# Kernel optimization log

Measured on AMD Instinct MI355X. Metric: run time of the kernel, lower is better.

Reference implementation:

```python
import jax, jax.numpy as jnp
import numpy as np
import math

B, L, E, H, D = 2, 2048, 2048, 16, 128
LOGIT_SCALE_MAX = math.log(1.0 / 0.01)
EPS = 1e-6


def rms_norm(x, scale, eps=EPS):
    # UIOLayerNorm: no mean subtraction, no bias, fp32 internals
    x32 = x.astype(jnp.float32)
    ms = jnp.mean(x32 * x32, axis=-1, keepdims=True)
    return (scale * (x32 * jax.lax.rsqrt(ms + eps)).astype(x.dtype)).astype(x.dtype)


def apply_rotary(x, rope):
    # x: [b, l, h, d]; rope: [b, l, d] interpreted as (cos, sin) interleaved pairs
    b, l, h, d = x.shape
    xr = x.astype(jnp.float32).reshape(b, l, h, d // 2, 2)
    rc = rope.astype(jnp.float32).reshape(b, l, 1, d // 2, 2)
    out = jnp.stack(
        [xr[..., 0] * rc[..., 0] - xr[..., 1] * rc[..., 1],
         xr[..., 1] * rc[..., 0] + xr[..., 0] * rc[..., 1]], axis=-1)
    return out.reshape(b, l, h, d).astype(x.dtype)


def l2_normalize(x, eps=1e-12):
    # matches F.normalize(dim=-1): x / max(||x||, eps)
    n = jnp.sqrt(jnp.sum(x * x, axis=-1, keepdims=True))
    return x / jnp.maximum(n, eps)


def setup_inputs() -> dict:
    key = jax.random.key(0)
    ks = jax.random.split(key, 12)
    scale = 1.0 / math.sqrt(E)
    return {
        "inputs_q": jax.random.normal(ks[0], (B, L, E), jnp.float32),
        "inputs_kv": jax.random.normal(ks[1], (B, L, E), jnp.float32),
        "bias": jax.random.normal(ks[2], (1, 1, L, L), jnp.float32),
        "q_sinusoids": jax.random.uniform(ks[3], (B, L, D), jnp.float32, -1.0, 1.0),
        "k_sinusoids": jax.random.uniform(ks[4], (B, L, D), jnp.float32, -1.0, 1.0),
        "Wq": jax.random.normal(ks[5], (E, E), jnp.float32) * scale,
        "Wk": jax.random.normal(ks[6], (E, E), jnp.float32) * scale,
        "Wv": jax.random.normal(ks[7], (E, E), jnp.float32) * scale,
        "Wo": jax.random.normal(ks[8], (E, E), jnp.float32) * scale,
        "q_norm_scale": jnp.ones((D,), jnp.float32),
        "k_norm_scale": jnp.ones((D,), jnp.float32),
        "logit_scale": jnp.full((H,), math.log(10.0), jnp.float32),
    }


def reference(inputs_q, inputs_kv, bias, q_sinusoids, k_sinusoids,
              Wq, Wk, Wv, Wo, q_norm_scale, k_norm_scale, logit_scale):
    dtype = inputs_q.dtype
    b, ql, e = inputs_q.shape
    kl = inputs_kv.shape[1]
    # QKV projections (nn.Linear, no bias), split heads -> [b, len, h, d]
    q = (inputs_q @ Wq.T).reshape(b, ql, H, D)
    k = (inputs_kv @ Wk.T).reshape(b, kl, H, D)
    v = (inputs_kv @ Wv.T).reshape(b, kl, H, D)
    # qk_norm (UIO RMS norm over head_dim)
    q = rms_norm(q, q_norm_scale)
    k = rms_norm(k, k_norm_scale)
    # RoPE
    q = apply_rotary(q, q_sinusoids)
    k = apply_rotary(k, k_sinusoids)
    # float32_logits
    q32 = q.astype(jnp.float32)
    k32 = k.astype(jnp.float32)
    # scaled cosine attention: L2-normalize q,k; learned per-head logit scale
    scores = jnp.einsum("bqhd,bkhd->bhqk", l2_normalize(q32), l2_normalize(k32))
    ls = jnp.exp(jnp.minimum(logit_scale, LOGIT_SCALE_MAX))
    scores = scores * ls[None, :, None, None]
    scores = scores + bias.astype(scores.dtype)
    attn = jax.nn.softmax(scores, axis=-1).astype(dtype)
    out = jnp.einsum("bhqk,bkhd->bqhd", attn, v)
    out = out.reshape(b, ql, e)
    return out @ Wo.T
```

## Files before the change

### kernel.cpp

```cpp
#include <hip/hip_runtime.h>
#include <hip/hip_bf16.h>

#define B_ 2
#define L_ 2048
#define E_ 2048
#define H_ 16
#define D_ 128
#define M_ (B_*L_)
#define LOGIT_SCALE_MAX_ 4.6051701859880914f
#define LOG2E_ 1.44269504088896f

typedef __bf16 bf16_t;
typedef __bf16 bf16x2 __attribute__((ext_vector_type(2)));
typedef __bf16 bf16x4 __attribute__((ext_vector_type(4)));
typedef __bf16 bf16x8 __attribute__((ext_vector_type(8)));
typedef float f32x4 __attribute__((ext_vector_type(4)));
typedef float f32x16 __attribute__((ext_vector_type(16)));

#define KSB(p, r, cb) ((p) * 32768 + (r) * 256 + ((cb) ^ (((r) & 7) << 4)))
#define VSB(p, r, cb) ((p) * 32768 + 16384 + (r) * 128 + ((cb) ^ (((r) & 7) << 4)))

#define NW_ 4194304L
#define NX_ 8388608L

__global__ void cvt_all_k(const float* __restrict__ xq, const float* __restrict__ xkv,
                          const float* __restrict__ bias,
                          const float* __restrict__ wq, const float* __restrict__ wk,
                          const float* __restrict__ wv, const float* __restrict__ wo,
                          bf16_t* __restrict__ ws) {
    const long NW4 = NW_ / 4, NX4 = NX_ / 4;
    long i4 = (long)blockIdx.x * 256 + threadIdx.x;
    const float* src; long off; float scale = 1.0f;
    if (i4 < 4 * NW4) {
        long r = i4 / NW4;
        src = (r == 0) ? wq : (r == 1) ? wk : (r == 2) ? wv : wo;
        off = i4 - r * NW4;
    } else if (i4 < 5 * NW4) {
        src = bias; off = i4 - 4 * NW4; scale = LOG2E_;
    } else if (i4 < 5 * NW4 + NX4) {
        src = xq; off = i4 - 5 * NW4;
    } else {
        src = xkv; off = i4 - 5 * NW4 - NX4;
    }
    float4 v = ((const float4*)src)[off];
    bf16x4 o = { (bf16_t)(v.x * scale), (bf16_t)(v.y * scale),
                 (bf16_t)(v.z * scale), (bf16_t)(v.w * scale) };
    ((bf16x4*)ws)[i4] = o;
}

template<typename OutT, int GROUPS>
__global__ __launch_bounds__(512, 2) void gemm8(
    const bf16_t* __restrict__ A0g, const bf16_t* __restrict__ A1g,
    const bf16_t* __restrict__ W0, OutT* __restrict__ C0) {
    __shared__ __align__(16) unsigned char smem[98304];
    const int tid = threadIdx.x;
    const int wid = tid >> 6, lane = tid & 63;
    const int fr = lane & 15, fq = lane >> 4;
    const int wm = wid & 3, wn = wid >> 2;
    int bid = blockIdx.x;
    { int cpx = (int)gridDim.x >> 3; bid = (bid & 7) * cpx + (bid >> 3); }
    const int g = (GROUPS > 1) ? (bid >> 8) : 0;
    const int wg = bid & 255;
    const int bm = wg >> 4, bn = wg & 15;
    const long arow0 = (long)bm * 256;
    const long brow0 = (long)bn * 128;
    const bf16_t* Ab = ((GROUPS > 1 && g > 0) ? A1g : A0g) + arow0 * E_;
    const bf16_t* Wb = W0 + (long)g * (long)E_ * E_ + brow0 * E_;

    f32x4 acc[4][4] = {};

    auto STAGE_A = [&](unsigned sbase, int kk, int j, int ktn_) {
        int row = j * 128 + (tid >> 2);
        int c16 = tid & 3;
        int col = kk * 32 + ((c16 ^ ((row >> 1) & 3)) * 8);
        __builtin_amdgcn_global_load_lds(
            (const __attribute__((address_space(1))) void*)(Ab + (long)row * E_ + ktn_ + col),
            (__attribute__((address_space(3))) void*)(smem + sbase + kk * 16384 + j * 8192 + tid * 16), 16, 0, 0);
    };
    auto STAGE_B = [&](unsigned sbase, int kk, int ktn_) {
        int row = tid >> 2;
        int c16 = tid & 3;
        int col = kk * 32 + ((c16 ^ ((row >> 1) & 3)) * 8);
        __builtin_amdgcn_global_load_lds(
            (const __attribute__((address_space(1))) void*)(Wb + (long)row * E_ + ktn_ + col),
            (__attribute__((address_space(3))) void*)(smem + sbase + 32768 + kk * 8192 + tid * 16), 16, 0, 0);
    };
    auto LDA = [&](unsigned pbase, int kk, int mi) -> bf16x8 {
        int row = wm * 64 + mi * 16 + fr;
        return *(const bf16x8*)(smem + pbase + kk * 16384 + row * 64 + ((fq ^ ((row >> 1) & 3)) << 4));
    };
    auto LDB = [&](unsigned pbase, int kk, int ni) -> bf16x8 {
        int row = wn * 64 + ni * 16 + fr;
        return *(const bf16x8*)(smem + pbase + 32768 + kk * 8192 + row * 64 + ((fq ^ ((row >> 1) & 3)) << 4));
    };

    STAGE_A(0, 0, 0, 0); STAGE_A(0, 0, 1, 0); STAGE_B(0, 0, 0);
    STAGE_A(0, 1, 0, 0); STAGE_A(0, 1, 1, 0); STAGE_B(0, 1, 0);
    asm volatile("s_waitcnt vmcnt(0)" ::: "memory");
    __builtin_amdgcn_s_barrier();

    #pragma unroll 2
    for (int t = 0; t < 32; ++t) {
        const unsigned pb = (unsigned)(t & 1) * 49152u;
        const unsigned sb = 49152u - pb;
        const int ktn = (t < 31) ? (t + 1) * 64 : 0;
        bf16x8 bq[4], a0, a1;
        a0 = LDA(pb, 0, 0); a1 = LDA(pb, 0, 1);
        bq[0] = LDB(pb, 0, 0); bq[1] = LDB(pb, 0, 1); bq[2] = LDB(pb, 0, 2); bq[3] = LDB(pb, 0, 3);
        STAGE_A(sb, 0, 0, ktn); STAGE_A(sb, 0, 1, ktn);
        __builtin_amdgcn_s_barrier();
        asm volatile("s_waitcnt lgkmcnt(0)" ::: "memory");
        __builtin_amdgcn_sched_barrier(0);
        __builtin_amdgcn_s_setprio(1);
        #pragma unroll
        for (int ni = 0; ni < 4; ++ni) {
            acc[0][ni] = __builtin_amdgcn_mfma_f32_16x16x32_bf16(a0, bq[ni], acc[0][ni], 0, 0, 0);
            acc[1][ni] = __builtin_amdgcn_mfma_f32_16x16x32_bf16(a1, bq[ni], acc[1][ni], 0, 0, 0);
        }
        __builtin_amdgcn_s_setprio(0);
        __builtin_amdgcn_s_barrier();
        a0 = LDA(pb, 0, 2); a1 = LDA(pb, 0, 3);
        STAGE_B(sb, 0, ktn);
        asm volatile("s_waitcnt vmcnt(3)" ::: "memory");
        __builtin_amdgcn_s_barrier();
        asm volatile("s_waitcnt lgkmcnt(0)" ::: "memory");
        __builtin_amdgcn_sched_barrier(0);
        __builtin_amdgcn_s_setprio(1);
        #pragma unroll
        for (int ni = 0; ni < 4; ++ni) {
            acc[2][ni] = __builtin_amdgcn_mfma_f32_16x16x32_bf16(a0, bq[ni], acc[2][ni], 0, 0, 0);
            acc[3][ni] = __builtin_amdgcn_mfma_f32_16x16x32_bf16(a1, bq[ni], acc[3][ni], 0, 0, 0);
        }
        __builtin_amdgcn_s_setprio(0);
        __builtin_amdgcn_s_barrier();
        a0 = LDA(pb, 1, 0); a1 = LDA(pb, 1, 1);
        bq[0] = LDB(pb, 1, 0); bq[1] = LDB(pb, 1, 1); bq[2] = LDB(pb, 1, 2); bq[3] = LDB(pb, 1, 3);
        STAGE_A(sb, 1, 0, ktn); STAGE_A(sb, 1, 1, ktn);
        __builtin_amdgcn_s_barrier();
        asm volatile("s_waitcnt lgkmcnt(0)" ::: "memory");
        __builtin_amdgcn_sched_barrier(0);
        __builtin_amdgcn_s_setprio(1);
        #pragma unroll
        for (int ni = 0; ni < 4; ++ni) {
            acc[0][ni] = __builtin_amdgcn_mfma_f32_16x16x32_bf16(a0, bq[ni], acc[0][ni], 0, 0, 0);
            acc[1][ni] = __builtin_amdgcn_mfma_f32_16x16x32_bf16(a1, bq[ni], acc[1][ni], 0, 0, 0);
        }
        __builtin_amdgcn_s_setprio(0);
        __builtin_amdgcn_s_barrier();
        a0 = LDA(pb, 1, 2); a1 = LDA(pb, 1, 3);
        STAGE_B(sb, 1, ktn);
        asm volatile("s_waitcnt vmcnt(3)" ::: "memory");
        __builtin_amdgcn_s_barrier();
        asm volatile("s_waitcnt lgkmcnt(0)" ::: "memory");
        __builtin_amdgcn_sched_barrier(0);
        __builtin_amdgcn_s_setprio(1);
        #pragma unroll
        for (int ni = 0; ni < 4; ++ni) {
            acc[2][ni] = __builtin_amdgcn_mfma_f32_16x16x32_bf16(a0, bq[ni], acc[2][ni], 0, 0, 0);
            acc[3][ni] = __builtin_amdgcn_mfma_f32_16x16x32_bf16(a1, bq[ni], acc[3][ni], 0, 0, 0);
        }
        __builtin_amdgcn_s_setprio(0);
        __builtin_amdgcn_s_barrier();
    }
    OutT* Cg = C0 + (long)g * M_ * E_;
    #pragma unroll
    for (int mi = 0; mi < 4; ++mi) {
        #pragma unroll
        for (int i = 0; i < 4; ++i) {
            long row = arow0 + wm * 64 + mi * 16 + fq * 4 + i;
            OutT* crow = Cg + row * E_ + brow0 + wn * 64 + fr;
            #pragma unroll
            for (int ni = 0; ni < 4; ++ni)
                crow[ni * 16] = (OutT)acc[mi][ni][i];
        }
    }
}

__global__ __launch_bounds__(256) void post_tv_k(
    const bf16_t* __restrict__ Pq, const bf16_t* __restrict__ Pk,
    const bf16_t* __restrict__ Vp,
    const float* __restrict__ qsins, const float* __restrict__ ksins,
    const float* __restrict__ qnscale, const float* __restrict__ knscale,
    bf16_t* __restrict__ outq, bf16_t* __restrict__ outk, bf16_t* __restrict__ Vt) {
    __shared__ bf16_t t[64 * 64];
    if (blockIdx.x < 32768) {
        const int wid = threadIdx.x >> 6, lane = threadIdx.x & 63;
        const int half = blockIdx.x >> 14;
        const long g = (long)(blockIdx.x & 16383) * 4 + wid;
        const bf16_t* P = half ? Pk : Pq;
        const float* sins = half ? ksins : qsins;
        const float* nscale = half ? knscale : qnscale;
        bf16_t* out = half ? outk : outq;
        const int h = (int)(g % H_);
        const long bl = g / H_;
        const int b = (int)(bl / L_), l = (int)(bl % L_);
        bf16x2 xv = *(const bf16x2*)(P + g * D_ + lane * 2);
        float x0 = (float)xv[0], x1 = (float)xv[1];
        float ss = x0 * x0 + x1 * x1;
        #pragma unroll
        for (int m = 1; m < 64; m <<= 1) ss += __shfl_xor(ss, m);
        float r = rsqrtf(ss * (1.0f / 128.0f) + 1e-6f);
        float y0 = x0 * r * nscale[lane * 2];
        float y1 = x1 * r * nscale[lane * 2 + 1];
        float2 cs = *(const float2*)(sins + bl * D_ + lane * 2);
        float z0 = y0 * cs.x - y1 * cs.y;
        float z1 = y1 * cs.x + y0 * cs.y;
        float n2 = z0 * z0 + z1 * z1;
        #pragma unroll
        for (int m = 1; m < 64; m <<= 1) n2 += __shfl_xor(n2, m);
        float inv = 1.0f / fmaxf(sqrtf(n2), 1e-12f);
        bf16x2 o = { (bf16_t)(z0 * inv), (bf16_t)(z1 * inv) };
        *(bf16x2*)(out + (((long)b * H_ + h) * L_ + l) * D_ + lane * 2) = o;
    } else {
        const int idx = blockIdx.x - 32768;
        const int lb = idx & 31;
        const int db = (idx >> 5) & 1;
        const int bh = idx >> 6;
        const int b = bh >> 4, h = bh & 15;
        const bf16_t* src = Vp + ((long)(b * L_ + lb * 64) * H_ + h) * D_ + db * 64;
        #pragma unroll
        for (int it = 0; it < 2; ++it) {
            int i = it * 256 + threadIdx.x;
            int r = i >> 3, c8 = i & 7;
            bf16x8 v = *(const bf16x8*)(src + (long)r * H_ * D_ + c8 * 8);
            *(bf16x8*)&t[r * 64 + (c8 ^ (r >> 3)) * 8] = v;
        }
        __syncthreads();
        bf16_t* dst = Vt + ((long)(b * H_ + h) * D_ + db * 64) * L_ + lb * 64;
        #pragma unroll
        for (int it = 0; it < 2; ++it) {
            int i = it * 256 + threadIdx.x;
            int d = i >> 3, l8 = i & 7;
            bf16x8 o;
            #pragma unroll
            for (int j = 0; j < 8; ++j) {
                int l = l8 * 8 + j;
                o[j] = t[l * 64 + ((d >> 3) ^ l8) * 8 + (d & 7)];
            }
            *(bf16x8*)(dst + (long)d * L_ + l8 * 8) = o;
        }
    }
}

__global__ __launch_bounds__(256, 2) void attn_k(
    const bf16_t* __restrict__ Qn, const bf16_t* __restrict__ Kn,
    const bf16_t* __restrict__ Vt, const bf16_t* __restrict__ biasb,
    const float* __restrict__ lsg, bf16_t* __restrict__ AO) {
    __shared__ __align__(16) unsigned char smem[65536];
    const int tid = threadIdx.x;
    const int w = tid >> 6, lane = tid & 63;
    const int lane31 = lane & 31, hi = lane >> 5;
    const int qb = blockIdx.x, bh = blockIdx.y;
    const int b = bh >> 4, h = bh & 15;
    const float lsc2 = __expf(fminf(lsg[h], LOGIT_SCALE_MAX_)) * LOG2E_;
    const int qr0 = qb * 128;
    const int qloc = w * 32 + lane31;
    const bf16_t* qrow  = Qn + (((long)b * H_ + h) * L_ + qr0 + qloc) * D_;
    const bf16_t* kbase = Kn + (((long)b * H_ + h) * L_) * D_;
    const bf16_t* vtbase = Vt + ((long)(b * H_ + h) * D_) * L_;
    const bf16_t* brow  = biasb + (long)(qr0 + qloc) * L_;

    const int ksr = tid >> 4, ksc = (tid & 15) * 8;
    const int vsr = tid >> 3, vsc = (tid & 7) * 8;

    bf16x8 qreg[8];
    #pragma unroll
    for (int kk = 0; kk < 8; ++kk)
        qreg[kk] = *(const bf16x8*)(qrow + kk * 16 + 8 * hi);

    f32x16 oacc[4] = {};
    float l_ = 0.f;

    bf16x8 kreg[4], vreg[4];
    #pragma unroll
    for (int it = 0; it < 4; ++it) {
        kreg[it] = *(const bf16x8*)(kbase + (long)(it * 16 + ksr) * D_ + ksc);
        vreg[it] = *(const bf16x8*)(vtbase + (long)(it * 32 + vsr) * L_ + vsc);
    }
    #pragma unroll
    for (int it = 0; it < 4; ++it) {
        *(bf16x8*)(smem + KSB(0, it * 16 + ksr, ksc * 2)) = kreg[it];
        *(bf16x8*)(smem + VSB(0, it * 32 + vsr, vsc * 2)) = vreg[it];
    }
    int p = 0;

    for (int kt = 0; kt < L_; kt += 64) {
        __syncthreads();
        const int ktn = (kt + 64 < L_) ? kt + 64 : 0;
        #pragma unroll
        for (int it = 0; it < 4; ++it) {
            kreg[it] = *(const bf16x8*)(kbase + (long)(ktn + it * 16 + ksr) * D_ + ksc);
            vreg[it] = *(const bf16x8*)(vtbase + (long)(it * 32 + vsr) * L_ + ktn + vsc);
        }
        bf16x4 bb[2][4];
        #pragma unroll
        for (int f = 0; f < 2; ++f)
            #pragma unroll
            for (int rr = 0; rr < 4; ++rr)
                bb[f][rr] = *(const bf16x4*)(brow + kt + f * 32 + rr * 8 + 4 * hi);
        f32x16 sacc[2] = {};
        __builtin_amdgcn_s_setprio(1);
        #pragma unroll
        for (int kk = 0; kk < 8; ++kk) {
            bf16x8 ak0 = *(const bf16x8*)(smem + KSB(p, lane31,      kk * 32 + 16 * hi));
            bf16x8 ak1 = *(const bf16x8*)(smem + KSB(p, 32 + lane31, kk * 32 + 16 * hi));
            sacc[0] = __builtin_amdgcn_mfma_f32_32x32x16_bf16(ak0, qreg[kk], sacc[0], 0, 0, 0);
            sacc[1] = __builtin_amdgcn_mfma_f32_32x32x16_bf16(ak1, qreg[kk], sacc[1], 0, 0, 0);
        }
        __builtin_amdgcn_s_setprio(0);
        float ps = 0.f;
        unsigned int wv[2][4][2];
        #pragma unroll
        for (int f = 0; f < 2; ++f)
            #pragma unroll
            for (int rr = 0; rr < 4; ++rr)
                #pragma unroll
                for (int wi = 0; wi < 2; ++wi) {
                    float pa = __builtin_amdgcn_exp2f(sacc[f][rr * 4 + wi * 2]     * lsc2 + (float)bb[f][rr][wi * 2]);
                    float pc = __builtin_amdgcn_exp2f(sacc[f][rr * 4 + wi * 2 + 1] * lsc2 + (float)bb[f][rr][wi * 2 + 1]);
                    ps += pa + pc;
                    bf16x2 t = { (bf16_t)pa, (bf16_t)pc };
                    wv[f][rr][wi] = __builtin_bit_cast(unsigned int, t);
                }
        ps += __shfl_xor(ps, 32);
        l_ += ps;
        bf16x8 pb_[4];
        #pragma unroll
        for (int kk = 0; kk < 4; ++kk) {
            const int f = kk >> 1;
            const int a2 = (kk & 1) * 2;
            unsigned int A0 = wv[f][a2][0],     A1 = wv[f][a2][1];
            unsigned int B0 = wv[f][a2 + 1][0], B1 = wv[f][a2 + 1][1];
            unsigned int own0  = hi ? B0 : A0;
            unsigned int own1  = hi ? B1 : A1;
            unsigned int send0 = hi ? A0 : B0;
            unsigned int send1 = hi ? A1 : B1;
            unsigned int recv0 = __shfl_xor(send0, 32);
            unsigned int recv1 = __shfl_xor(send1, 32);
            uint4 uu;
            uu.x = hi ? recv0 : own0;
            uu.y = hi ? recv1 : own1;
            uu.z = hi ? own0  : recv0;
            uu.w = hi ? own1  : recv1;
            pb_[kk] = __builtin_bit_cast(bf16x8, uu);
        }
        __builtin_amdgcn_s_setprio(1);
        #pragma unroll
        for (int df = 0; df < 4; ++df)
            #pragma unroll
            for (int kk = 0; kk < 4; ++kk) {
                bf16x8 av = *(const bf16x8*)(smem + VSB(p, df * 32 + lane31, kk * 32 + 16 * hi));
                oacc[df] = __builtin_amdgcn_mfma_f32_32x32x16_bf16(av, pb_[kk], oacc[df], 0, 0, 0);
            }
        __builtin_amdgcn_s_setprio(0);
        if (kt + 64 < L_) {
            #pragma unroll
            for (int it = 0; it < 4; ++it) {
                *(bf16x8*)(smem + KSB(p ^ 1, it * 16 + ksr, ksc * 2)) = kreg[it];
                *(bf16x8*)(smem + VSB(p ^ 1, it * 32 + vsr, vsc * 2)) = vreg[it];
            }
        }
        p ^= 1;
    }
    __syncthreads();
    float inv = 1.0f / l_;
    #pragma unroll
    for (int df = 0; df < 4; ++df)
        #pragma unroll
        for (int rg = 0; rg < 16; ++rg) {
            int d = df * 32 + (rg & 3) + 8 * (rg >> 2) + 4 * hi;
            *(bf16_t*)(smem + qloc * 264 + d * 2) = (bf16_t)(oacc[df][rg] * inv);
        }
    __syncthreads();
    #pragma unroll
    for (int it = 0; it < 8; ++it) {
        int idx = it * 256 + tid;
        int row = idx >> 4, c = idx & 15;
        bf16x8 v = *(const bf16x8*)(smem + row * 264 + c * 16);
        *(bf16x8*)(AO + ((long)b * L_ + qr0 + row) * E_ + h * D_ + c * 8) = v;
    }
}

extern "C" void kernel_launch(void* const* d_in, const int* in_sizes, int n_in,
                              void* d_out, int out_size, void* d_ws, size_t ws_size,
                              hipStream_t stream) {
    const float* inputs_q  = (const float*)d_in[0];
    const float* inputs_kv = (const float*)d_in[1];
    const float* bias      = (const float*)d_in[2];
    const float* q_sin     = (const float*)d_in[3];
    const float* k_sin     = (const float*)d_in[4];
    const float* Wq        = (const float*)d_in[5];
    const float* Wk        = (const float*)d_in[6];
    const float* Wv        = (const float*)d_in[7];
    const float* Wo        = (const float*)d_in[8];
    const float* qns       = (const float*)d_in[9];
    const float* kns       = (const float*)d_in[10];
    const float* lsg       = (const float*)d_in[11];

    bf16_t* ws = (bf16_t*)d_ws;
    const long NW = NW_;
    const long NX = NX_;
    bf16_t* Wq_b   = ws;
    bf16_t* Wo_b   = ws + 3 * NW;
    bf16_t* bias_b = ws + 4 * NW;
    bf16_t* Xq     = bias_b + NW;
    bf16_t* Xkv    = Xq + NX;
    bf16_t* Qp     = Xkv + NX;
    bf16_t* Kp     = Qp + NX;
    bf16_t* Vp     = Kp + NX;
    bf16_t* Qn = Xq;
    bf16_t* Kn = Xkv;
    bf16_t* AO = Qp;
    bf16_t* Vtr = Kp;
    if (ws_size < (size_t)(5 * NW + 5 * NX) * 2) return;

    {
        long n4 = (5 * NW + 2 * NX) / 4;
        cvt_all_k<<<dim3((unsigned)(n4 / 256)), dim3(256), 0, stream>>>(
            inputs_q, inputs_kv, bias, Wq, Wk, Wv, Wo, ws);
    }

    gemm8<bf16_t, 3><<<dim3(768), dim3(512), 0, stream>>>(Xq, Xkv, Wq_b, Qp);

    post_tv_k<<<dim3(34816), dim3(256), 0, stream>>>(
        Qp, Kp, Vp, q_sin, k_sin, qns, kns, Qn, Kn, Vtr);

    attn_k<<<dim3(L_ / 128, B_ * H_), dim3(256), 0, stream>>>(Qn, Kn, Vtr, bias_b, lsg, AO);

    gemm8<float, 1><<<dim3(256), dim3(512), 0, stream>>>(AO, AO, Wo_b, (float*)d_out);
}
```

Measured before the change: 320.0 us.

## Use 256x256 output tiles for the fused QKV projection GEMM

Adds a new GEMM kernel for the QKV projections with 256x256 tiles, 128 KB of shared memory and a double-buffered 64-wide K step. A and B loads are staggered across four MFMA phases. The QKV launch drops from 768 to 384 workgroups, raising arithmetic intensity per tile and cutting global/L2 traffic for re-reading A and W. The old 256x128 kernel is kept, specialised, for the output projection. The risks are lower occupancy from 128 KB LDS (likely one block per CU despite launch bounds of 2), higher accumulator register pressure, and fewer workgroups to fill the CUs.

```diff
diff --git a/kernel.cpp b/kernel.cpp
--- a/kernel.cpp
+++ b/kernel.cpp
@@ -49,9 +49,150 @@
 }
 
 template<typename OutT, int GROUPS>
-__global__ __launch_bounds__(512, 2) void gemm8(
+__global__ __launch_bounds__(512, 2) void gemm256(
     const bf16_t* __restrict__ A0g, const bf16_t* __restrict__ A1g,
     const bf16_t* __restrict__ W0, OutT* __restrict__ C0) {
+    __shared__ __align__(16) unsigned char smem[131072];
+    const int tid = threadIdx.x;
+    const int wid = tid >> 6, lane = tid & 63;
+    const int fr = lane & 15, fq = lane >> 4;
+    const int wm = wid >> 2, wn = wid & 3;
+    int bid = blockIdx.x;
+    { int cpx = (int)gridDim.x >> 3; bid = (bid & 7) * cpx + (bid >> 3); }
+    const int g = (GROUPS > 1) ? (bid >> 7) : 0;
+    const int wg = (GROUPS > 1) ? (bid & 127) : bid;
+    const int bm = wg >> 3, bn = wg & 7;
+    const long arow0 = (long)bm * 256;
+    const long brow0 = (long)bn * 256;
+    const bf16_t* Ab = ((GROUPS > 1 && g > 0) ? A1g : A0g) + arow0 * E_;
+    const bf16_t* Wb = W0 + (long)g * (long)E_ * E_ + brow0 * E_;
+
+    f32x4 acc[8][4] = {};
+
+    const int srow = tid >> 2;
+    const int sc16 = tid & 3;
+    auto STG = [&](const bf16_t* base, unsigned matOff, int h, unsigned bufb, int kt) {
+        #pragma unroll
+        for (int kk = 0; kk < 2; ++kk) {
+            int col = kk * 32 + ((sc16 ^ ((srow >> 1) & 3)) * 8);
+            __builtin_amdgcn_global_load_lds(
+                (const __attribute__((address_space(1))) void*)(base + (long)(h * 128 + srow) * E_ + kt + col),
+                (__attribute__((address_space(3))) void*)(smem + bufb + matOff + h * 16384u + kk * 8192u + tid * 16), 16, 0, 0);
+        }
+    };
+    auto LDA = [&](unsigned pb, int kk, int mi) -> bf16x8 {
+        int r = wm * 128 + mi * 16 + fr;
+        int lr = r & 127;
+        return *(const bf16x8*)(smem + pb + (unsigned)(r >> 7) * 16384u + kk * 8192u + lr * 64 + ((fq ^ ((lr >> 1) & 3)) << 4));
+    };
+    auto LDB = [&](unsigned pb, int kk, int ni) -> bf16x8 {
+        int r = wn * 64 + ni * 16 + fr;
+        int lr = r & 127;
+        return *(const bf16x8*)(smem + pb + 32768u + (unsigned)(r >> 7) * 16384u + kk * 8192u + lr * 64 + ((fq ^ ((lr >> 1) & 3)) << 4));
+    };
+
+    STG(Ab, 0u,     0, 0u, 0); STG(Ab, 0u,     1, 0u, 0);
+    STG(Wb, 32768u, 0, 0u, 0); STG(Wb, 32768u, 1, 0u, 0);
+    STG(Wb, 32768u, 0, 65536u, 64); STG(Wb, 32768u, 1, 65536u, 64);
+    asm volatile("s_waitcnt vmcnt(4)" ::: "memory");
+    __builtin_amdgcn_s_barrier();
+
+    bf16x8 bq[2][4];
+    #pragma unroll 2
+    for (int t = 0; t < 32; ++t) {
+        const unsigned pb = (unsigned)(t & 1) * 65536u;
+        const unsigned sbA = 65536u - pb;
+        const int ktA = ((t + 1) & 31) * 64;
+        const int ktB = ((t + 2) & 31) * 64;
+        bf16x8 a[2][2];
+        #pragma unroll
+        for (int kk = 0; kk < 2; ++kk) {
+            a[kk][0] = LDA(pb, kk, 0); a[kk][1] = LDA(pb, kk, 1);
+            #pragma unroll
+            for (int ni = 0; ni < 4; ++ni) bq[kk][ni] = LDB(pb, kk, ni);
+        }
+        STG(Ab, 0u, 0, sbA, ktA);
+        __builtin_amdgcn_s_barrier();
+        asm volatile("s_waitcnt lgkmcnt(0)" ::: "memory");
+        __builtin_amdgcn_sched_barrier(0);
+        __builtin_amdgcn_s_setprio(1);
+        #pragma unroll
+        for (int kk = 0; kk < 2; ++kk)
+            #pragma unroll
+            for (int ni = 0; ni < 4; ++ni) {
+                acc[0][ni] = __builtin_amdgcn_mfma_f32_16x16x32_bf16(a[kk][0], bq[kk][ni], acc[0][ni], 0, 0, 0);
+                acc[1][ni] = __builtin_amdgcn_mfma_f32_16x16x32_bf16(a[kk][1], bq[kk][ni], acc[1][ni], 0, 0, 0);
+            }
+        __builtin_amdgcn_s_setprio(0);
+        __builtin_amdgcn_s_barrier();
+        #pragma unroll
+        for (int kk = 0; kk < 2; ++kk) { a[kk][0] = LDA(pb, kk, 2); a[kk][1] = LDA(pb, kk, 3); }
+        STG(Ab, 0u, 1, sbA, ktA);
+        __builtin_amdgcn_s_barrier();
+        asm volatile("s_waitcnt lgkmcnt(0)" ::: "memory");
+        __builtin_amdgcn_sched_barrier(0);
+        __builtin_amdgcn_s_setprio(1);
+        #pragma unroll
+        for (int kk = 0; kk < 2; ++kk)
+            #pragma unroll
+            for (int ni = 0; ni < 4; ++ni) {
+                acc[2][ni] = __builtin_amdgcn_mfma_f32_16x16x32_bf16(a[kk][0], bq[kk][ni], acc[2][ni], 0, 0, 0);
+                acc[3][ni] = __builtin_amdgcn_mfma_f32_16x16x32_bf16(a[kk][1], bq[kk][ni], acc[3][ni], 0, 0, 0);
+            }
+        __builtin_amdgcn_s_setprio(0);
+        __builtin_amdgcn_s_barrier();
+        #pragma unroll
+        for (int kk = 0; kk < 2; ++kk) { a[kk][0] = LDA(pb, kk, 4); a[kk][1] = LDA(pb, kk, 5); }
+        STG(Wb, 32768u, 0, pb, ktB);
+        __builtin_amdgcn_s_barrier();
+        asm volatile("s_waitcnt lgkmcnt(0)" ::: "memory");
+        __builtin_amdgcn_sched_barrier(0);
+        __builtin_amdgcn_s_setprio(1);
+        #pragma unroll
+        for (int kk = 0; kk < 2; ++kk)
+            #pragma unroll
+            for (int ni = 0; ni < 4; ++ni) {
+                acc[4][ni] = __builtin_amdgcn_mfma_f32_16x16x32_bf16(a[kk][0], bq[kk][ni], acc[4][ni], 0, 0, 0);
+                acc[5][ni] = __builtin_amdgcn_mfma_f32_16x16x32_bf16(a[kk][1], bq[kk][ni], acc[5][ni], 0, 0, 0);
+            }
+        __builtin_amdgcn_s_setprio(0);
+        __builtin_amdgcn_s_barrier();
+        #pragma unroll
+        for (int kk = 0; kk < 2; ++kk) { a[kk][0] = LDA(pb, kk, 6); a[kk][1] = LDA(pb, kk, 7); }
+        STG(Wb, 32768u, 1, pb, ktB);
+        asm volatile("s_waitcnt vmcnt(4)" ::: "memory");
+        __builtin_amdgcn_s_barrier();
+        asm volatile("s_waitcnt lgkmcnt(0)" ::: "memory");
+        __builtin_amdgcn_sched_barrier(0);
+        __builtin_amdgcn_s_setprio(1);
+        #pragma unroll
+        for (int kk = 0; kk < 2; ++kk)
+            #pragma unroll
+            for (int ni = 0; ni < 4; ++ni) {
+                acc[6][ni] = __builtin_amdgcn_mfma_f32_16x16x32_bf16(a[kk][0], bq[kk][ni], acc[6][ni], 0, 0, 0);
+                acc[7][ni] = __builtin_amdgcn_mfma_f32_16x16x32_bf16(a[kk][1], bq[kk][ni], acc[7][ni], 0, 0, 0);
+            }
+        __builtin_amdgcn_s_setprio(0);
+        __builtin_amdgcn_s_barrier();
+    }
+    asm volatile("s_waitcnt vmcnt(0)" ::: "memory");
+    OutT* Cg = C0 + (long)g * M_ * E_;
+    #pragma unroll
+    for (int mi = 0; mi < 8; ++mi) {
+        #pragma unroll
+        for (int i = 0; i < 4; ++i) {
+            long row = arow0 + wm * 128 + mi * 16 + fq * 4 + i;
+            OutT* crow = Cg + row * E_ + brow0 + wn * 64 + fr;
+            #pragma unroll
+            for (int ni = 0; ni < 4; ++ni)
+                crow[ni * 16] = (OutT)acc[mi][ni][i];
+        }
+    }
+}
+
+template<typename OutT>
+__global__ __launch_bounds__(512, 2) void gemm8o(
+    const bf16_t* __restrict__ A0g, const bf16_t* __restrict__ W0, OutT* __restrict__ C0) {
     __shared__ __align__(16) unsigned char smem[98304];
     const int tid = threadIdx.x;
     const int wid = tid >> 6, lane = tid & 63;
@@ -59,13 +200,11 @@
     const int wm = wid & 3, wn = wid >> 2;
     int bid = blockIdx.x;
     { int cpx = (int)gridDim.x >> 3; bid = (bid & 7) * cpx + (bid >> 3); }
-    const int g = (GROUPS > 1) ? (bid >> 8) : 0;
-    const int wg = bid & 255;
-    const int bm = wg >> 4, bn = wg & 15;
+    const int bm = bid >> 4, bn = bid & 15;
     const long arow0 = (long)bm * 256;
     const long brow0 = (long)bn * 128;
-    const bf16_t* Ab = ((GROUPS > 1 && g > 0) ? A1g : A0g) + arow0 * E_;
-    const bf16_t* Wb = W0 + (long)g * (long)E_ * E_ + brow0 * E_;
+    const bf16_t* Ab = A0g + arow0 * E_;
+    const bf16_t* Wb = W0 + brow0 * E_;
 
     f32x4 acc[4][4] = {};
 
@@ -162,13 +301,12 @@
         __builtin_amdgcn_s_setprio(0);
         __builtin_amdgcn_s_barrier();
     }
-    OutT* Cg = C0 + (long)g * M_ * E_;
     #pragma unroll
     for (int mi = 0; mi < 4; ++mi) {
         #pragma unroll
         for (int i = 0; i < 4; ++i) {
             long row = arow0 + wm * 64 + mi * 16 + fq * 4 + i;
-            OutT* crow = Cg + row * E_ + brow0 + wn * 64 + fr;
+            OutT* crow = C0 + row * E_ + brow0 + wn * 64 + fr;
             #pragma unroll
             for (int ni = 0; ni < 4; ++ni)
                 crow[ni * 16] = (OutT)acc[mi][ni][i];
@@ -420,12 +558,12 @@
             inputs_q, inputs_kv, bias, Wq, Wk, Wv, Wo, ws);
     }
 
-    gemm8<bf16_t, 3><<<dim3(768), dim3(512), 0, stream>>>(Xq, Xkv, Wq_b, Qp);
+    gemm256<bf16_t, 3><<<dim3(384), dim3(512), 0, stream>>>(Xq, Xkv, Wq_b, Qp);
 
     post_tv_k<<<dim3(34816), dim3(256), 0, stream>>>(
         Qp, Kp, Vp, q_sin, k_sin, qns, kns, Qn, Kn, Vtr);
 
     attn_k<<<dim3(L_ / 128, B_ * H_), dim3(256), 0, stream>>>(Qn, Kn, Vtr, bias_b, lsg, AO);
 
-    gemm8<float, 1><<<dim3(256), dim3(512), 0, stream>>>(AO, AO, Wo_b, (float*)d_out);
+    gemm8o<float><<<dim3(256), dim3(512), 0, stream>>>(AO, Wo_b, (float*)d_out);
 }
```

Result: faster. 311.1 us (-2.8%).
